# Performance work log

Hardware: AMD Instinct MI355X
Metric: run time of the kernel (lower is better)

Reference implementation:

```python
import jax, jax.numpy as jnp
import numpy as np

B, S, E, H = 4, 2048, 1024, 16
D = E // H  # head_dim = 64


def setup_inputs() -> dict:
    key = jax.random.key(0)
    ks = jax.random.split(key, 10)
    scale = 1.0 / np.sqrt(E)
    return {
        "decoder_sequence": jax.random.normal(ks[0], (B, S, E), dtype=jnp.float32),
        # stacked per-head projection weights (math-equivalent to per-head nn.Linear)
        "Wq": jax.random.normal(ks[1], (H, E, D), dtype=jnp.float32) * scale,
        "bq": jnp.zeros((H, D), dtype=jnp.float32),
        "Wk": jax.random.normal(ks[2], (H, E, D), dtype=jnp.float32) * scale,
        "bk": jnp.zeros((H, D), dtype=jnp.float32),
        "Wv": jax.random.normal(ks[3], (H, E, D), dtype=jnp.float32) * scale,
        "bv": jnp.zeros((H, D), dtype=jnp.float32),
        "Wo": jax.random.normal(ks[4], (E, E), dtype=jnp.float32) * scale,
        "bo": jnp.zeros((E,), dtype=jnp.float32),
    }


def reference(decoder_sequence, Wq, bq, Wk, bk, Wv, bv, Wo, bo):
    x = decoder_sequence  # [B,S,E]
    # per-head Q/K/V projections, batched over the head axis
    Q = jnp.einsum('bse,hed->bhsd', x, Wq) + bq[:, None, :]
    K = jnp.einsum('bse,hed->bhsd', x, Wk) + bk[:, None, :]
    V = jnp.einsum('bse,hed->bhsd', x, Wv) + bv[:, None, :]
    # scaled scores with causal mask (upper triangle -> -inf)
    A = jnp.einsum('bhid,bhjd->bhij', Q, K) / jnp.sqrt(jnp.float32(D))
    causal = jnp.tril(jnp.ones((S, S), dtype=bool))  # True where allowed
    A = jnp.where(causal, A, -jnp.inf)
    A = jax.nn.softmax(A, axis=-1)
    Hout = jnp.einsum('bhij,bhjd->bhid', A, V)  # [B,H,S,D]
    # concat heads: [B,S,H*D]
    concat = jnp.transpose(Hout, (0, 2, 1, 3)).reshape(B, S, H * D)
    return concat @ Wo.T + bo
```

## Files before the change

kernel.cpp:

```cpp
#include <hip/hip_runtime.h>
#include <stdint.h>
#include <stddef.h>

typedef __bf16 bf16;
typedef __bf16 bf16x8 __attribute__((ext_vector_type(8)));
typedef __bf16 bf16x4 __attribute__((ext_vector_type(4)));
typedef float  f32x4  __attribute__((ext_vector_type(4)));
typedef float  f32x16 __attribute__((ext_vector_type(16)));
typedef unsigned short ush;
typedef ush ush8 __attribute__((ext_vector_type(8)));
typedef unsigned int uint;

#define B_  4
#define S_  2048
#define E_  1024
#define H_  16
#define D_  64
#define M_  (B_*S_)
#define K_  E_
#define QSCALE 0.18033688011112042f
#define SSHIFT 16.0f

__device__ __forceinline__ void gload_lds16(const void* g, void* l) {
  __builtin_amdgcn_global_load_lds((const __attribute__((address_space(1))) void*)g,
                                   (__attribute__((address_space(3))) void*)l, 16, 0, 0);
}
__device__ __forceinline__ f32x4 mfma16(bf16x8 a, bf16x8 b, f32x4 c) {
  return __builtin_amdgcn_mfma_f32_16x16x32_bf16(a, b, c, 0, 0, 0);
}
__device__ __forceinline__ f32x16 mfma32(bf16x8 a, bf16x8 b, f32x16 c) {
  return __builtin_amdgcn_mfma_f32_32x32x16_bf16(a, b, c, 0, 0, 0);
}
__device__ __forceinline__ int swz4(int row, int ch) { return ch ^ ((row >> 1) & 3); }
__device__ __forceinline__ uint cvtpk(float lo, float hi) {
  uint r;
  asm("v_cvt_pk_bf16_f32 %0, %1, %2" : "=v"(r) : "v"(lo), "v"(hi));
  return r;
}

__global__ void fused_cast(const float* __restrict__ x, bf16* __restrict__ Xbf,
                           const float* __restrict__ Wo, bf16* __restrict__ Wot) {
  const int n4x = (M_ * K_) / 4, n4w = (E_ * E_) / 4;
  int idx = blockIdx.x * blockDim.x + threadIdx.x;
  int stride = gridDim.x * blockDim.x;
  for (int i = idx; i < n4x + n4w; i += stride) {
    const float4 v = (i < n4x) ? ((const float4*)x)[i] : ((const float4*)Wo)[i - n4x];
    union { bf16 b[4]; ushort4 u; } cv;
    cv.b[0] = (bf16)v.x; cv.b[1] = (bf16)v.y; cv.b[2] = (bf16)v.z; cv.b[3] = (bf16)v.w;
    if (i < n4x) ((ushort4*)Xbf)[i] = cv.u;
    else         ((ushort4*)Wot)[i - n4x] = cv.u;
  }
}

__global__ void pack_w_t(const float* __restrict__ Wq, const float* __restrict__ Wk,
                         const float* __restrict__ Wv, bf16* __restrict__ Wp) {
  __shared__ float t[64][65];
  const int tid = threadIdx.x;
  const int wh = blockIdx.y;
  const int which = wh >> 4, h = wh & 15;
  const int e0 = blockIdx.x << 6;
  const float* src = (which == 0) ? Wq : (which == 1 ? Wk : Wv);
  src += (size_t)h * (E_ * D_);
  #pragma unroll
  for (int i = 0; i < 4; ++i) {
    int fi = tid + 256 * i;
    int e = fi >> 4, c = fi & 15;
    float4 v = *(const float4*)(src + (size_t)(e0 + e) * D_ + c * 4);
    t[c * 4 + 0][e] = v.x; t[c * 4 + 1][e] = v.y;
    t[c * 4 + 2][e] = v.z; t[c * 4 + 3][e] = v.w;
  }
  __syncthreads();
  #pragma unroll
  for (int i = 0; i < 2; ++i) {
    int cid = tid + 256 * i;
    int d = cid >> 3, cc = cid & 7;
    ush8 o;
    #pragma unroll
    for (int j = 0; j < 8; ++j) {
      union { bf16 b; ush u; } cv; cv.b = (bf16)t[d][cc * 8 + j]; o[j] = cv.u;
    }
    *(ush8*)(Wp + ((size_t)which * 1024 + h * 64 + d) * K_ + e0 + cc * 8) = o;
  }
}

template <int MODE>
__launch_bounds__(256, 3)
__global__ void gemm_kernel(const bf16* __restrict__ A, const bf16* __restrict__ Bm,
                            int Ntot,
                            const float* __restrict__ bias0, const float* __restrict__ bias1,
                            const float* __restrict__ bias2,
                            bf16* __restrict__ Qo, bf16* __restrict__ Ko, bf16* __restrict__ Vto,
                            float* __restrict__ Fo) {
  __shared__ __align__(16) bf16 lds_a[2][128 * 32];
  __shared__ __align__(16) bf16 lds_b[2][128 * 32];
  const int tid = threadIdx.x;
  const int lane = tid & 63;
  const int w = tid >> 6;
  const int wr = w >> 1, wc = w & 1;
  const int nblk = Ntot >> 7;
  const int qch = gridDim.x >> 3;
  const int swz = (blockIdx.x & 7) * qch + (blockIdx.x >> 3);
  const int mt = swz / nblk, nt = swz % nblk;
  const int m0 = mt << 7, n0 = nt << 7;

  f32x4 acc[4][4] = {};

  auto stage = [&](int buf, int kt) {
    #pragma unroll
    for (int i = 0; i < 2; ++i) {
      int cb = (w * 2 + i) * 64;
      int cid = cb + lane;
      int row = cid >> 2, cir = cid & 3;
      int lch = swz4(row, cir);
      const bf16* ga = A  + (size_t)(m0 + row) * K_ + kt * 32 + lch * 8;
      const bf16* gb = Bm + (size_t)(n0 + row) * K_ + kt * 32 + lch * 8;
      gload_lds16(ga, &lds_a[buf][cb * 8]);
      gload_lds16(gb, &lds_b[buf][cb * 8]);
    }
  };

  const int NT = K_ / 32;
  stage(0, 0);
  for (int kt = 0; kt < NT; ++kt) {
    if (kt + 1 < NT) stage((kt + 1) & 1, kt + 1);
    __syncthreads();
    const bf16x8* pa = (const bf16x8*)&lds_a[kt & 1][0];
    const bf16x8* pb = (const bf16x8*)&lds_b[kt & 1][0];
    bf16x8 af[4], bfr[4];
    #pragma unroll
    for (int mb = 0; mb < 4; ++mb) {
      int row = wr * 64 + mb * 16 + (lane & 15);
      af[mb] = pa[row * 4 + swz4(row, lane >> 4)];
    }
    #pragma unroll
    for (int nb = 0; nb < 4; ++nb) {
      int row = wc * 64 + nb * 16 + (lane & 15);
      bfr[nb] = pb[row * 4 + swz4(row, lane >> 4)];
    }
    #pragma unroll
    for (int mb = 0; mb < 4; ++mb)
      #pragma unroll
      for (int nb = 0; nb < 4; ++nb)
        acc[mb][nb] = mfma16(af[mb], bfr[nb], acc[mb][nb]);
    __syncthreads();
  }

  #pragma unroll
  for (int mb = 0; mb < 4; ++mb) {
    #pragma unroll
    for (int nb = 0; nb < 4; ++nb) {
      const int ni  = n0 + wc * 64 + nb * 16 + (lane & 15);
      const int mi0 = m0 + wr * 64 + mb * 16 + (lane >> 4) * 4;
      if (MODE == 0) {
        const int which = ni >> 10;
        const int col = ni & 1023;
        const float* bp = (which == 0) ? bias0 : (which == 1 ? bias1 : bias2);
        const float bv = bp[col];
        const int hh = col >> 6, d = col & 63;
        const int b = mi0 >> 11, s0r = mi0 & 2047;
        if (which == 2) {
          bf16x4 st;
          #pragma unroll
          for (int r = 0; r < 4; ++r) st[r] = (bf16)(acc[mb][nb][r] + bv);
          *(bf16x4*)(Vto + ((size_t)((b * H_ + hh) * D_ + d)) * S_ + s0r) = st;
        } else {
          bf16* dst = (which == 0) ? Qo : Ko;
          const float sc = (which == 0) ? QSCALE : 1.f;
          #pragma unroll
          for (int r = 0; r < 4; ++r)
            dst[(((size_t)(b * H_ + hh)) * S_ + (s0r + r)) * D_ + d] =
                (bf16)((acc[mb][nb][r] + bv) * sc);
        }
      } else {
        #pragma unroll
        for (int r = 0; r < 4; ++r)
          Fo[(size_t)(mi0 + r) * E_ + ni] = acc[mb][nb][r] + bias0[ni];
      }
    }
  }
}

struct QTile {
  bf16x8 qf[4];
  f32x16 oacc[2];
  float l;
};
struct KVF {
  bf16x8 k0[4], k1[4];
  bf16x8 v0[4], v1[4];
};

__device__ __forceinline__ void init_q(QTile& S, const bf16* qrow, int hi) {
  #pragma unroll
  for (int kc = 0; kc < 4; ++kc)
    S.qf[kc] = *(const bf16x8*)(qrow + (2 * kc + hi) * 8);
  #pragma unroll
  for (int r = 0; r < 16; ++r) { S.oacc[0][r] = 0.f; S.oacc[1][r] = 0.f; }
  S.l = 0.f;
}

__device__ __forceinline__ void load_frags(KVF& F, const bf16* klds, const bf16* vlds,
                                           int sub, int hi, int ln) {
  const bf16* kbase = klds + sub * (64 * 64);
  const int lxor = (ln & 7) ^ ((ln >> 3) & 3);
  #pragma unroll
  for (int kc = 0; kc < 4; ++kc) {
    int ch = (2 * kc + hi) ^ lxor;
    F.k0[kc] = *(const bf16x8*)&kbase[ln * 64 + ch * 8];
    F.k1[kc] = *(const bf16x8*)&kbase[(32 + ln) * 64 + ch * 8];
  }
  #pragma unroll
  for (int ks = 0; ks < 4; ++ks) {
    int cf = sub * 8 + 2 * ks + hi;
    int ch = cf ^ (ln & 15);
    F.v0[ks] = *(const bf16x8*)&vlds[ln * 128 + ch * 8];
    F.v1[ks] = *(const bf16x8*)&vlds[(32 + ln) * 128 + ch * 8];
  }
}

__device__ __forceinline__ void step_one(QTile& S, const KVF& F,
                                         int kv0, int qb_, int qg_, int hi) {
  if (kv0 > qb_ + 31) return;
  f32x16 s0 = {}, s1 = {};
  __builtin_amdgcn_s_setprio(1);
  #pragma unroll
  for (int kc = 0; kc < 4; ++kc) {
    s0 = mfma32(F.k0[kc], S.qf[kc], s0);
    s1 = mfma32(F.k1[kc], S.qf[kc], s1);
  }
  __builtin_amdgcn_s_setprio(0);
  if (kv0 + 63 > qb_) {
    #pragma unroll
    for (int r = 0; r < 16; ++r) {
      int crow = (r & 3) + 8 * (r >> 2) + 4 * hi;
      if (kv0 + crow > qg_)      s0[r] = -1e30f;
      if (kv0 + 32 + crow > qg_) s1[r] = -1e30f;
    }
  }
  #pragma unroll
  for (int r = 0; r < 16; ++r) {
    s0[r] = exp2f(s0[r] - SSHIFT);
    s1[r] = exp2f(s1[r] - SSHIFT);
  }
  bf16x8 pf[4];
  #pragma unroll
  for (int mtl = 0; mtl < 2; ++mtl) {
    #pragma unroll
    for (int c = 0; c < 2; ++c) {
      const f32x16& p = mtl ? s1 : s0;
      uint wa = cvtpk(p[8 * c + 0], p[8 * c + 1]);
      uint wb = cvtpk(p[8 * c + 2], p[8 * c + 3]);
      uint wcx = cvtpk(p[8 * c + 4], p[8 * c + 5]);
      uint wd = cvtpk(p[8 * c + 6], p[8 * c + 7]);
      asm("v_permlane32_swap_b32 %0, %1" : "+v"(wa), "+v"(wcx));
      asm("v_permlane32_swap_b32 %0, %1" : "+v"(wb), "+v"(wd));
      union { uint u[4]; bf16x8 v; } cvt;
      cvt.u[0] = wa; cvt.u[1] = wb; cvt.u[2] = wcx; cvt.u[3] = wd;
      pf[mtl * 2 + c] = cvt.v;
    }
  }
  const bf16 one_ = (bf16)1.f;
  const bf16x8 vones = {one_, one_, one_, one_, one_, one_, one_, one_};
  f32x16 lt = {};
  __builtin_amdgcn_s_setprio(1);
  #pragma unroll
  for (int ks = 0; ks < 4; ++ks) lt = mfma32(vones, pf[ks], lt);
  #pragma unroll
  for (int ks = 0; ks < 4; ++ks) {
    S.oacc[0] = mfma32(F.v0[ks], pf[ks], S.oacc[0]);
    S.oacc[1] = mfma32(F.v1[ks], pf[ks], S.oacc[1]);
  }
  __builtin_amdgcn_s_setprio(0);
  S.l += lt[0];
}

__device__ __forceinline__ void store_o(const QTile& S, bf16* orow, int hi) {
  float rinv = 1.f / S.l;
  #pragma unroll
  for (int dm = 0; dm < 2; ++dm) {
    #pragma unroll
    for (int g = 0; g < 4; ++g) {
      bf16x4 st;
      #pragma unroll
      for (int i = 0; i < 4; ++i) st[i] = (bf16)(S.oacc[dm][4 * g + i] * rinv);
      *(bf16x4*)(orow + dm * 32 + g * 8 + hi * 4) = st;
    }
  }
}

__launch_bounds__(256, 2)
__global__ void attn_kernel(const bf16* __restrict__ Q, const bf16* __restrict__ K,
                            const bf16* __restrict__ Vt, bf16* __restrict__ Cc) {
  __shared__ __align__(16) bf16 k_lds[2][128 * 64];
  __shared__ __align__(16) bf16 v_lds[2][64 * 128];
  const int tid = threadIdx.x, lane = tid & 63, w = tid >> 6;
  const int hi = lane >> 5, ln = lane & 31;
  const int bid = blockIdx.x;
  const int bh = bid & 63;
  const int x = bid >> 6;
  const bf16* Kb = K  + (size_t)bh * (S_ * D_);
  const bf16* Vb = Vt + (size_t)bh * (D_ * S_);
  const int b = bh >> 4, hh = bh & 15;

  const int qbA = x * 128 + w * 32,        qgA = qbA + ln;
  const int qbB = (15 - x) * 128 + w * 32, qgB = qbB + ln;
  const int nphA = x + 1, nphB = 16 - x;

  QTile SA, SB;
  init_q(SA, Q + ((size_t)bh * S_ + qgA) * D_, hi);
  init_q(SB, Q + ((size_t)bh * S_ + qgB) * D_, hi);

  auto stage2 = [&](int buf, int ph) {
    const int kv0 = ph << 7;
    #pragma unroll
    for (int i = 0; i < 4; ++i) {
      int cb = (w * 4 + i) * 64;
      int cid = cb + lane;
      int row = cid >> 3, cir = cid & 7;
      int lch = cir ^ (row & 7) ^ ((row >> 3) & 3);
      gload_lds16(Kb + (size_t)(kv0 + row) * D_ + lch * 8, &k_lds[buf][cb * 8]);
      int rowv = cid >> 4, cirv = cid & 15;
      int lchv = cirv ^ (rowv & 15);
      gload_lds16(Vb + (size_t)rowv * S_ + kv0 + lchv * 8, &v_lds[buf][cb * 8]);
    }
  };

  stage2(0, 0);
  __syncthreads();
  for (int ph = 0; ph < nphB; ++ph) {
    const int cur = ph & 1;
    if (ph + 1 < nphB) stage2(cur ^ 1, ph + 1);
    const int kv0 = ph << 7;
    {
      KVF F0;
      load_frags(F0, k_lds[cur], v_lds[cur], 0, hi, ln);
      if (ph < nphA) step_one(SA, F0, kv0, qbA, qgA, hi);
      step_one(SB, F0, kv0, qbB, qgB, hi);
    }
    {
      KVF F1;
      load_frags(F1, k_lds[cur], v_lds[cur], 1, hi, ln);
      if (ph < nphA) step_one(SA, F1, kv0 + 64, qbA, qgA, hi);
      step_one(SB, F1, kv0 + 64, qbB, qgB, hi);
    }
    __syncthreads();
  }

  store_o(SA, Cc + ((size_t)(b * S_ + qgA)) * E_ + hh * D_, hi);
  store_o(SB, Cc + ((size_t)(b * S_ + qgB)) * E_ + hh * D_, hi);
}

extern "C" void kernel_launch(void* const* d_in, const int* in_sizes, int n_in,
                              void* d_out, int out_size, void* d_ws, size_t ws_size,
                              hipStream_t stream) {
  const float* x  = (const float*)d_in[0];
  const float* Wq = (const float*)d_in[1];
  const float* bq = (const float*)d_in[2];
  const float* Wk = (const float*)d_in[3];
  const float* bk = (const float*)d_in[4];
  const float* Wv = (const float*)d_in[5];
  const float* bv = (const float*)d_in[6];
  const float* Wo = (const float*)d_in[7];
  const float* bo = (const float*)d_in[8];
  float* out = (float*)d_out;

  uint8_t* ws = (uint8_t*)d_ws;
  bf16* Xbf   = (bf16*)(ws + 0);
  bf16* Wpack = (bf16*)(ws + 16777216);
  bf16* Wot   = (bf16*)(ws + 23068672);
  bf16* Qb    = (bf16*)(ws + 25165824);
  bf16* Kb    = (bf16*)(ws + 41943040);
  bf16* Vtb   = (bf16*)(ws + 75497472);
  bf16* Cc    = Xbf;

  fused_cast<<<2048, 256, 0, stream>>>(x, Xbf, Wo, Wot);
  pack_w_t<<<dim3(16, 48), 256, 0, stream>>>(Wq, Wk, Wv, Wpack);

  gemm_kernel<0><<<dim3(64 * 24), 256, 0, stream>>>(Xbf, Wpack, 3072, bq, bk, bv,
                                                    Qb, Kb, Vtb, nullptr);

  attn_kernel<<<dim3(512), 256, 0, stream>>>(Qb, Kb, Vtb, Cc);

  gemm_kernel<1><<<dim3(64 * 8), 256, 0, stream>>>(Cc, Wot, 1024, bo, nullptr, nullptr,
                                                   nullptr, nullptr, nullptr, out);
}
```

Measured before the change: 181.8 us.

## Use 128x256 GEMM tiles with 8 waves and a 4-stage LDS pipeline

Replaces the 128x128, 4-wave GEMM with a 128x256 tile computed by 8 waves per block. Global-to-LDS loads now run three stages ahead with explicit vmcnt waits instead of double buffering, and MFMA issue is bracketed with s_setprio. The goal is to hide global load latency and improve operand reuse in both projection GEMMs. In exchange it uses much more LDS per block (96 KB), which limits occupancy, and the grid gets smaller (256 blocks for the output GEMM).

```diff
diff --git a/kernel.cpp b/kernel.cpp
--- a/kernel.cpp
+++ b/kernel.cpp
@@ -84,73 +84,83 @@
 }
 
 template <int MODE>
-__launch_bounds__(256, 3)
-__global__ void gemm_kernel(const bf16* __restrict__ A, const bf16* __restrict__ Bm,
-                            int Ntot,
-                            const float* __restrict__ bias0, const float* __restrict__ bias1,
-                            const float* __restrict__ bias2,
-                            bf16* __restrict__ Qo, bf16* __restrict__ Ko, bf16* __restrict__ Vto,
-                            float* __restrict__ Fo) {
-  __shared__ __align__(16) bf16 lds_a[2][128 * 32];
-  __shared__ __align__(16) bf16 lds_b[2][128 * 32];
+__launch_bounds__(512, 2)
+__global__ void gemm256(const bf16* __restrict__ A, const bf16* __restrict__ Bm,
+                        int nblk,
+                        const float* __restrict__ bias0, const float* __restrict__ bias1,
+                        const float* __restrict__ bias2,
+                        bf16* __restrict__ Qo, bf16* __restrict__ Ko, bf16* __restrict__ Vto,
+                        float* __restrict__ Fo) {
+  __shared__ __align__(16) bf16 a_lds[4][128 * 32];
+  __shared__ __align__(16) bf16 b_lds[4][256 * 32];
   const int tid = threadIdx.x;
   const int lane = tid & 63;
-  const int w = tid >> 6;
-  const int wr = w >> 1, wc = w & 1;
-  const int nblk = Ntot >> 7;
+  const int wid = tid >> 6;
+  const int wr = wid >> 2, wc = wid & 3;
   const int qch = gridDim.x >> 3;
-  const int swz = (blockIdx.x & 7) * qch + (blockIdx.x >> 3);
+  const int swz = ((int)blockIdx.x & 7) * qch + ((int)blockIdx.x >> 3);
   const int mt = swz / nblk, nt = swz % nblk;
-  const int m0 = mt << 7, n0 = nt << 7;
+  const int m0 = mt << 7, n0 = nt << 8;
 
   f32x4 acc[4][4] = {};
 
-  auto stage = [&](int buf, int kt) {
-    #pragma unroll
-    for (int i = 0; i < 2; ++i) {
-      int cb = (w * 2 + i) * 64;
-      int cid = cb + lane;
+  auto stage = [&](int kt) {
+    const int buf = kt & 3;
+    {
+      int cid = tid;
       int row = cid >> 2, cir = cid & 3;
       int lch = swz4(row, cir);
-      const bf16* ga = A  + (size_t)(m0 + row) * K_ + kt * 32 + lch * 8;
-      const bf16* gb = Bm + (size_t)(n0 + row) * K_ + kt * 32 + lch * 8;
-      gload_lds16(ga, &lds_a[buf][cb * 8]);
-      gload_lds16(gb, &lds_b[buf][cb * 8]);
+      gload_lds16(A + (size_t)(m0 + row) * K_ + kt * 32 + lch * 8, &a_lds[buf][cid * 8]);
+    }
+    #pragma unroll
+    for (int u = 0; u < 2; ++u) {
+      int cid = u * 512 + tid;
+      int row = cid >> 2, cir = cid & 3;
+      int lch = swz4(row, cir);
+      gload_lds16(Bm + (size_t)(n0 + row) * K_ + kt * 32 + lch * 8, &b_lds[buf][cid * 8]);
     }
   };
 
   const int NT = K_ / 32;
-  stage(0, 0);
+  stage(0); stage(1); stage(2);
   for (int kt = 0; kt < NT; ++kt) {
-    if (kt + 1 < NT) stage((kt + 1) & 1, kt + 1);
-    __syncthreads();
-    const bf16x8* pa = (const bf16x8*)&lds_a[kt & 1][0];
-    const bf16x8* pb = (const bf16x8*)&lds_b[kt & 1][0];
+    if (kt + 3 < NT) stage(kt + 3);
+    if      (kt + 3 < NT) asm volatile("s_waitcnt vmcnt(9)" ::: "memory");
+    else if (kt + 2 < NT) asm volatile("s_waitcnt vmcnt(6)" ::: "memory");
+    else if (kt + 1 < NT) asm volatile("s_waitcnt vmcnt(3)" ::: "memory");
+    else                  asm volatile("s_waitcnt vmcnt(0)" ::: "memory");
+    __builtin_amdgcn_s_barrier();
+    __builtin_amdgcn_sched_barrier(0);
+    const int buf = kt & 3;
+    const bf16x8* pa = (const bf16x8*)&a_lds[buf][0];
+    const bf16x8* pb = (const bf16x8*)&b_lds[buf][0];
     bf16x8 af[4], bfr[4];
     #pragma unroll
-    for (int mb = 0; mb < 4; ++mb) {
-      int row = wr * 64 + mb * 16 + (lane & 15);
-      af[mb] = pa[row * 4 + swz4(row, lane >> 4)];
-    }
-    #pragma unroll
-    for (int nb = 0; nb < 4; ++nb) {
-      int row = wc * 64 + nb * 16 + (lane & 15);
-      bfr[nb] = pb[row * 4 + swz4(row, lane >> 4)];
-    }
-    #pragma unroll
-    for (int mb = 0; mb < 4; ++mb)
+    for (int i = 0; i < 4; ++i) {
+      int row = wr * 64 + i * 16 + (lane & 15);
+      af[i] = pa[row * 4 + swz4(row, lane >> 4)];
+    }
+    #pragma unroll
+    for (int j = 0; j < 4; ++j) {
+      int row = wc * 64 + j * 16 + (lane & 15);
+      bfr[j] = pb[row * 4 + swz4(row, lane >> 4)];
+    }
+    __builtin_amdgcn_s_setprio(1);
+    #pragma unroll
+    for (int i = 0; i < 4; ++i)
       #pragma unroll
-      for (int nb = 0; nb < 4; ++nb)
-        acc[mb][nb] = mfma16(af[mb], bfr[nb], acc[mb][nb]);
-    __syncthreads();
-  }
-
-  #pragma unroll
-  for (int mb = 0; mb < 4; ++mb) {
-    #pragma unroll
-    for (int nb = 0; nb < 4; ++nb) {
-      const int ni  = n0 + wc * 64 + nb * 16 + (lane & 15);
-      const int mi0 = m0 + wr * 64 + mb * 16 + (lane >> 4) * 4;
+      for (int j = 0; j < 4; ++j)
+        acc[i][j] = mfma16(af[i], bfr[j], acc[i][j]);
+    __builtin_amdgcn_s_setprio(0);
+    __builtin_amdgcn_s_barrier();
+  }
+
+  #pragma unroll
+  for (int i = 0; i < 4; ++i) {
+    #pragma unroll
+    for (int j = 0; j < 4; ++j) {
+      const int ni  = n0 + wc * 64 + j * 16 + (lane & 15);
+      const int mi0 = m0 + wr * 64 + i * 16 + (lane >> 4) * 4;
       if (MODE == 0) {
         const int which = ni >> 10;
         const int col = ni & 1023;
@@ -161,7 +171,7 @@
         if (which == 2) {
           bf16x4 st;
           #pragma unroll
-          for (int r = 0; r < 4; ++r) st[r] = (bf16)(acc[mb][nb][r] + bv);
+          for (int r = 0; r < 4; ++r) st[r] = (bf16)(acc[i][j][r] + bv);
           *(bf16x4*)(Vto + ((size_t)((b * H_ + hh) * D_ + d)) * S_ + s0r) = st;
         } else {
           bf16* dst = (which == 0) ? Qo : Ko;
@@ -169,12 +179,12 @@
           #pragma unroll
           for (int r = 0; r < 4; ++r)
             dst[(((size_t)(b * H_ + hh)) * S_ + (s0r + r)) * D_ + d] =
-                (bf16)((acc[mb][nb][r] + bv) * sc);
+                (bf16)((acc[i][j][r] + bv) * sc);
         }
       } else {
         #pragma unroll
         for (int r = 0; r < 4; ++r)
-          Fo[(size_t)(mi0 + r) * E_ + ni] = acc[mb][nb][r] + bias0[ni];
+          Fo[(size_t)(mi0 + r) * E_ + ni] = acc[i][j][r] + bias0[ni];
       }
     }
   }
@@ -376,11 +386,11 @@
   fused_cast<<<2048, 256, 0, stream>>>(x, Xbf, Wo, Wot);
   pack_w_t<<<dim3(16, 48), 256, 0, stream>>>(Wq, Wk, Wv, Wpack);
 
-  gemm_kernel<0><<<dim3(64 * 24), 256, 0, stream>>>(Xbf, Wpack, 3072, bq, bk, bv,
-                                                    Qb, Kb, Vtb, nullptr);
+  gemm256<0><<<dim3(768), 512, 0, stream>>>(Xbf, Wpack, 12, bq, bk, bv,
+                                            Qb, Kb, Vtb, nullptr);
 
   attn_kernel<<<dim3(512), 256, 0, stream>>>(Qb, Kb, Vtb, Cc);
 
-  gemm_kernel<1><<<dim3(64 * 8), 256, 0, stream>>>(Cc, Wot, 1024, bo, nullptr, nullptr,
-                                                   nullptr, nullptr, nullptr, out);
-}
+  gemm256<1><<<dim3(256), 512, 0, stream>>>(Cc, Wot, 4, bo, nullptr, nullptr,
+                                            nullptr, nullptr, nullptr, out);
+}
```

Result: slower. 202.2 us (+11.2%).
